# Optimization experiments

Measured on AMD Instinct MI355X. Metric: run time of the kernel, lower is better.

The kernel has to match this reference:

```python
import jax, jax.numpy as jnp
import numpy as np

NUM_HEADS = 16


def setup_inputs() -> dict:
    key = jax.random.key(0)
    k1, k2, k3 = jax.random.split(key, 3)
    B, S, D = 4, 2048, 1024
    x = jax.random.normal(k1, (B, S, D), dtype=jnp.float32)
    w_qkv = jax.random.normal(k2, (D, 3 * D), dtype=jnp.float32) * 0.02
    b_qkv = jnp.zeros((3 * D,), dtype=jnp.float32)
    w_proj = jax.random.normal(k3, (D, D), dtype=jnp.float32) * 0.02
    b_proj = jnp.zeros((D,), dtype=jnp.float32)
    return {"x": x, "w_qkv": w_qkv, "b_qkv": b_qkv, "w_proj": w_proj, "b_proj": b_proj}


def reference(x, w_qkv, b_qkv, w_proj, b_proj):
    B, S, D = x.shape
    H = NUM_HEADS
    hd = D // H
    # fused qkv projection: [B,S,3D] -> [B,S,3H,hd]
    qkv = (x @ w_qkv + b_qkv).reshape(B, S, 3 * H, hd)
    q, k, v = jnp.split(qkv, 3, axis=2)  # each [B,S,H,hd]
    scale = (1.0 / jnp.sqrt(hd)).astype(x.dtype)
    scores = jnp.einsum("bqhd,bkhd->bhqk", q, k) * scale  # [B,H,S,S]
    causal = jnp.tril(jnp.ones((S, S), dtype=bool))  # [S,S]
    masked = jnp.where(causal, scores, jnp.finfo(scores.dtype).min)
    # softmax in fp32 reduce dtype, cast back (dropout_rate=0 -> identity)
    attn = jax.nn.softmax(masked.astype(jnp.float32)).astype(masked.dtype)
    out = jnp.einsum("bhqk,bkhd->bqhd", attn, v).reshape(B, S, D)
    return out @ w_proj + b_proj
```

## Files before the change

kernel.cpp:

```cpp
#include <hip/hip_runtime.h>
#include <hip/hip_bf16.h>

typedef __attribute__((ext_vector_type(8))) short short8;
typedef __attribute__((ext_vector_type(4))) float f32x4;
typedef __attribute__((ext_vector_type(16))) float f32x16;

#define B_   4
#define S_   2048
#define D_   1024
#define H_   16
#define HD_  64
#define M_   (B_ * S_)
#define N3_  (3 * D_)

#define GLDS16(g, l)                                                        \
  __builtin_amdgcn_global_load_lds(                                         \
      (const __attribute__((address_space(1))) void*)(g),                   \
      (__attribute__((address_space(3))) void*)(l), 16, 0, 0)

__device__ __forceinline__ unsigned pack_bf2(float a, float b) {
  union { __hip_bfloat16 h; unsigned short s; } ua, ub;
  ua.h = __float2bfloat16(a);
  ub.h = __float2bfloat16(b);
  return (unsigned)ua.s | ((unsigned)ub.s << 16);
}

__global__ __launch_bounds__(256) void cast_f32_bf16(
    const float* __restrict__ in, __hip_bfloat16* __restrict__ out, int n) {
  int i = (blockIdx.x * 256 + threadIdx.x) * 4;
  if (i + 3 < n) {
    float4 v = *(const float4*)(in + i);
    union { ushort4 u4; __hip_bfloat16 h[4]; } p;
    p.h[0] = __float2bfloat16(v.x);
    p.h[1] = __float2bfloat16(v.y);
    p.h[2] = __float2bfloat16(v.z);
    p.h[3] = __float2bfloat16(v.w);
    *(ushort4*)(out + i) = p.u4;
  }
}

__global__ __launch_bounds__(256) void transpose_cast(
    const float* __restrict__ in, __hip_bfloat16* __restrict__ out,
    int rows, int cols) {
  __shared__ float tile[32][33];
  int bx = blockIdx.x * 32;
  int by = blockIdx.y * 32;
  int tx = threadIdx.x, ty = threadIdx.y;
#pragma unroll
  for (int i = 0; i < 4; ++i)
    tile[ty + i * 8][tx] = in[(size_t)(by + ty + i * 8) * cols + bx + tx];
  __syncthreads();
#pragma unroll
  for (int i = 0; i < 4; ++i)
    out[(size_t)(bx + ty + i * 8) * rows + by + tx] =
        __float2bfloat16(tile[tx][ty + i * 8]);
}

__device__ inline void store_out(float* p, float v) { *p = v; }
__device__ inline void store_out(__hip_bfloat16* p, float v) {
  *p = __float2bfloat16(v);
}

template <typename OUT_T, bool WVT>
__global__ __launch_bounds__(256) void gemm_bt_bias(
    const __hip_bfloat16* __restrict__ A, const __hip_bfloat16* __restrict__ Bt,
    const float* __restrict__ bias, OUT_T* __restrict__ C,
    __hip_bfloat16* __restrict__ vt, int M, int N, int K) {
  __shared__ __align__(16) __hip_bfloat16 Alds[128 * 64];
  __shared__ __align__(16) __hip_bfloat16 Blds[128 * 64];
  const int t = threadIdx.x;
  const int wave = t >> 6, lane = t & 63;
  const int quad = lane >> 4, l15 = lane & 15;
  const int wm = (wave >> 1) * 64, wn = (wave & 1) * 64;
  const int m0 = blockIdx.y * 128, n0 = blockIdx.x * 128;

  const int rsub = lane >> 3;
  const int gc16 = (lane & 7) ^ (rsub & 7);
  const __hip_bfloat16* gA[4];
  const __hip_bfloat16* gB[4];
  __hip_bfloat16* lA[4];
  __hip_bfloat16* lB[4];
#pragma unroll
  for (int i = 0; i < 4; ++i) {
    int c = wave * 4 + i;
    int row = c * 8 + rsub;
    gA[i] = A + (size_t)(m0 + row) * K + gc16 * 8;
    gB[i] = Bt + (size_t)(n0 + row) * K + gc16 * 8;
    lA[i] = Alds + c * 512;
    lB[i] = Blds + c * 512;
  }

  f32x4 acc[4][4] = {};

  for (int k0 = 0; k0 < K; k0 += 64) {
#pragma unroll
    for (int i = 0; i < 4; ++i) {
      GLDS16(gA[i] + k0, lA[i]);
      GLDS16(gB[i] + k0, lB[i]);
    }
    __syncthreads();
#pragma unroll
    for (int kk = 0; kk < 2; ++kk) {
      const int fo = ((kk * 4 + quad) ^ (l15 & 7)) * 8;
      short8 a[4], bfr[4];
#pragma unroll
      for (int mt = 0; mt < 4; ++mt)
        a[mt] = *(const short8*)(Alds + (wm + mt * 16 + l15) * 64 + fo);
#pragma unroll
      for (int nt = 0; nt < 4; ++nt)
        bfr[nt] = *(const short8*)(Blds + (wn + nt * 16 + l15) * 64 + fo);
#pragma unroll
      for (int mt = 0; mt < 4; ++mt)
#pragma unroll
        for (int nt = 0; nt < 4; ++nt)
          acc[mt][nt] = __builtin_amdgcn_mfma_f32_16x16x32_bf16(
              a[mt], bfr[nt], acc[mt][nt], 0, 0, 0);
    }
    __syncthreads();
  }

  if (WVT && n0 >= 2048) {
#pragma unroll
    for (int mt = 0; mt < 4; ++mt)
#pragma unroll
      for (int nt = 0; nt < 4; ++nt) {
        int col = n0 + wn + nt * 16 + l15;
        float bv = bias[col];
        int hv = (col - 2048) >> 6, d = (col - 2048) & 63;
        int row0 = m0 + wm + mt * 16 + quad * 4;
        int bidx = row0 >> 11, s = row0 & 2047;
        uint2 w;
        w.x = pack_bf2(acc[mt][nt][0] + bv, acc[mt][nt][1] + bv);
        w.y = pack_bf2(acc[mt][nt][2] + bv, acc[mt][nt][3] + bv);
        *(uint2*)(vt + ((size_t)(bidx * 16 + hv) * 64 + d) * 2048 + s) = w;
      }
  } else {
#pragma unroll
    for (int mt = 0; mt < 4; ++mt)
#pragma unroll
      for (int nt = 0; nt < 4; ++nt) {
        int col = n0 + wn + nt * 16 + l15;
        float bv = bias[col];
#pragma unroll
        for (int r = 0; r < 4; ++r) {
          int row = m0 + wm + mt * 16 + quad * 4 + r;
          store_out(C + (size_t)row * N + col, acc[mt][nt][r] + bv);
        }
      }
  }
}

__global__ __launch_bounds__(128, 2) void attn_causal(
    const __hip_bfloat16* __restrict__ qkv,
    const __hip_bfloat16* __restrict__ vt,
    __hip_bfloat16* __restrict__ ctx) {
  __shared__ __align__(16) __hip_bfloat16 Klds[2][64 * 64];
  __shared__ __align__(16) __hip_bfloat16 Vlds[2][64 * 64];

  const int t = threadIdx.x;
  const int wave = t >> 6, lane = t & 63;
  const int r31 = lane & 31, a5 = lane >> 5;
  const int xr = r31 & 7;

  const int wg = blockIdx.x;
  const int xcd = wg & 7, loc = wg >> 3;
  const int pair = (xcd << 3) | (loc >> 4);
  const int xb = loc & 15;
  const int b = pair >> 4, h = pair & 15;

  const size_t qbase = (size_t)b * S_ * N3_ + h * HD_;
  const size_t kbase = qbase + D_;
  const size_t vtbase = (size_t)(b * H_ + h) * HD_ * S_;
  const float C2 = 0.18033688f;

  short8 ones;
#pragma unroll
  for (int j = 0; j < 8; ++j) ones[j] = (short)0x3F80;

  const int rsub = lane >> 3;
  const int swz = ((lane & 7) ^ rsub) * 8;
  const __hip_bfloat16* gK[4];
  const __hip_bfloat16* gV[4];
  __hip_bfloat16* lK[4];
  __hip_bfloat16* lV[4];
#pragma unroll
  for (int i = 0; i < 4; ++i) {
    const int c = wave * 4 + i;
    gK[i] = qkv + kbase + (size_t)(c * 8 + rsub) * N3_ + swz;
    gV[i] = vt + vtbase + (size_t)(c * 8 + rsub) * S_ + swz;
    lK[i] = &Klds[0][c * 512];
    lV[i] = &Vlds[0][c * 512];
  }

#pragma unroll
  for (int i = 0; i < 4; ++i) {
    GLDS16(gK[i], lK[i]);
    GLDS16(gV[i], lV[i]);
  }
  __syncthreads();
  int cur = 0;

#define MKFRAG(sv, Bofs, OUT)                                          \
  {                                                                    \
    unsigned dA0 = pack_bf2(sv[Bofs + 0], sv[Bofs + 1]);               \
    unsigned dA1 = pack_bf2(sv[Bofs + 2], sv[Bofs + 3]);               \
    unsigned dB0 = pack_bf2(sv[Bofs + 4], sv[Bofs + 5]);               \
    unsigned dB1 = pack_bf2(sv[Bofs + 6], sv[Bofs + 7]);               \
    unsigned c0 = (unsigned)__shfl_xor((int)(a5 ? dA0 : dB0), 32);     \
    unsigned c1 = (unsigned)__shfl_xor((int)(a5 ? dA1 : dB1), 32);     \
    union { unsigned u[4]; short8 s8; } pu;                            \
    pu.u[0] = a5 ? c0 : dA0;                                           \
    pu.u[1] = a5 ? c1 : dA1;                                           \
    pu.u[2] = a5 ? dB0 : c0;                                           \
    pu.u[3] = a5 ? dB1 : c1;                                           \
    OUT = pu.s8;                                                       \
  }

  for (int sel = 0; sel < 2; ++sel) {
    const int qb = sel ? 31 - xb : xb;
    const int qrow = qb * 64 + wave * 32 + r31;
    const int rlq = wave * 32 + r31;

    short8 qf[4];
#pragma unroll
    for (int dc = 0; dc < 4; ++dc)
      qf[dc] = *(const short8*)(qkv + qbase + (size_t)qrow * N3_ +
                                dc * 16 + a5 * 8);

    f32x16 o0 = {}, o1 = {};
    float m_r = -1e30f, l_r = 0.f;

    for (int kb = 0; kb <= qb; ++kb) {
      if (sel == 0 || kb < qb) {
        const size_t nk = (kb < qb) ? (size_t)(kb + 1) : 0;
        const size_t ko = nk * (size_t)(64 * N3_);
        const size_t vo = nk * 64;
        const int nb = (cur ^ 1) * 4096;
#pragma unroll
        for (int i = 0; i < 4; ++i) {
          GLDS16(gK[i] + ko, lK[i] + nb);
          GLDS16(gV[i] + vo, lV[i] + nb);
        }
      }

      const __hip_bfloat16* Kb = &Klds[cur][0];
      const __hip_bfloat16* Vb = &Vlds[cur][0];

      short8 kf0[4], kf1[4];
#pragma unroll
      for (int dc = 0; dc < 4; ++dc) {
        const int u = ((dc * 2 + a5) ^ xr) * 8;
        kf0[dc] = *(const short8*)(Kb + r31 * 64 + u);
        kf1[dc] = *(const short8*)(Kb + (32 + r31) * 64 + u);
      }

      f32x16 s0 = {}, s1 = {};
#pragma unroll
      for (int dc = 0; dc < 4; ++dc) {
        s0 = __builtin_amdgcn_mfma_f32_32x32x16_bf16(kf0[dc], qf[dc], s0,
                                                     0, 0, 0);
        s1 = __builtin_amdgcn_mfma_f32_32x32x16_bf16(kf1[dc], qf[dc], s1,
                                                     0, 0, 0);
      }

      if (kb == qb) {
#pragma unroll
        for (int reg = 0; reg < 16; ++reg) {
          const int kl = (reg & 3) + 8 * (reg >> 2) + 4 * a5;
          if (kl > rlq) s0[reg] = -1e30f;
          if (kl + 32 > rlq) s1[reg] = -1e30f;
        }
      }

      float tm = s0[0];
#pragma unroll
      for (int reg = 1; reg < 16; ++reg) tm = fmaxf(tm, s0[reg]);
#pragma unroll
      for (int reg = 0; reg < 16; ++reg) tm = fmaxf(tm, s1[reg]);
      tm = fmaxf(tm, __shfl_xor(tm, 32));
      const float pm = tm * C2;

      if (!__all(pm - m_r <= 8.0f)) {
        const float mn = fmaxf(m_r, pm);
        const float al = __builtin_amdgcn_exp2f(m_r - mn);
        m_r = mn;
        l_r *= al;
        o0 *= al;
        o1 *= al;
      }
      const float mneg = -m_r;

#pragma unroll
      for (int reg = 0; reg < 16; ++reg) {
        s0[reg] = __builtin_amdgcn_exp2f(__builtin_fmaf(s0[reg], C2, mneg));
        s1[reg] = __builtin_amdgcn_exp2f(__builtin_fmaf(s1[reg], C2, mneg));
      }

      short8 pf[4];
      MKFRAG(s0, 0, pf[0]);
      MKFRAG(s0, 8, pf[1]);
      MKFRAG(s1, 0, pf[2]);
      MKFRAG(s1, 8, pf[3]);

      f32x16 ps = {};
#pragma unroll
      for (int kc = 0; kc < 4; ++kc)
        ps = __builtin_amdgcn_mfma_f32_32x32x16_bf16(ones, pf[kc], ps,
                                                     0, 0, 0);
      l_r += ps[0];

#pragma unroll
      for (int kc = 0; kc < 4; ++kc) {
        const int u = ((kc * 2 + a5) ^ xr) * 8;
        short8 v0 = *(const short8*)(Vb + r31 * 64 + u);
        short8 v1 = *(const short8*)(Vb + (32 + r31) * 64 + u);
        o0 = __builtin_amdgcn_mfma_f32_32x32x16_bf16(v0, pf[kc], o0, 0, 0, 0);
        o1 = __builtin_amdgcn_mfma_f32_32x32x16_bf16(v1, pf[kc], o1, 0, 0, 0);
      }

      __syncthreads();
      cur ^= 1;
    }

    const float rl = __builtin_amdgcn_rcpf(l_r);
    __hip_bfloat16* crow = ctx + ((size_t)b * S_ + qrow) * D_ + h * HD_;
#pragma unroll
    for (int q2 = 0; q2 < 4; ++q2) {
      uint2 w;
      w.x = pack_bf2(o0[q2 * 4 + 0] * rl, o0[q2 * 4 + 1] * rl);
      w.y = pack_bf2(o0[q2 * 4 + 2] * rl, o0[q2 * 4 + 3] * rl);
      *(uint2*)(crow + 8 * q2 + 4 * a5) = w;
      w.x = pack_bf2(o1[q2 * 4 + 0] * rl, o1[q2 * 4 + 1] * rl);
      w.y = pack_bf2(o1[q2 * 4 + 2] * rl, o1[q2 * 4 + 3] * rl);
      *(uint2*)(crow + 32 + 8 * q2 + 4 * a5) = w;
    }
  }
#undef MKFRAG
}

extern "C" void kernel_launch(void* const* d_in, const int* in_sizes, int n_in,
                              void* d_out, int out_size, void* d_ws,
                              size_t ws_size, hipStream_t stream) {
  const float* x      = (const float*)d_in[0];
  const float* w_qkv  = (const float*)d_in[1];
  const float* b_qkv  = (const float*)d_in[2];
  const float* w_proj = (const float*)d_in[3];
  const float* b_proj = (const float*)d_in[4];
  float* out = (float*)d_out;

  char* ws = (char*)d_ws;
  __hip_bfloat16* xb     = (__hip_bfloat16*)(ws + 0);
  __hip_bfloat16* wqkvT  = (__hip_bfloat16*)(ws + 16777216);
  __hip_bfloat16* wprojT = (__hip_bfloat16*)(ws + 23068672);
  __hip_bfloat16* qkvb   = (__hip_bfloat16*)(ws + 25165824);
  __hip_bfloat16* ctx    = (__hip_bfloat16*)(ws + 75497472);
  __hip_bfloat16* vt2    = (__hip_bfloat16*)(ws + 91750400);

  cast_f32_bf16<<<8192, 256, 0, stream>>>(x, xb, M_ * D_);
  transpose_cast<<<dim3(N3_ / 32, D_ / 32), dim3(32, 8), 0, stream>>>(
      w_qkv, wqkvT, D_, N3_);
  transpose_cast<<<dim3(D_ / 32, D_ / 32), dim3(32, 8), 0, stream>>>(
      w_proj, wprojT, D_, D_);

  gemm_bt_bias<__hip_bfloat16, true>
      <<<dim3(N3_ / 128, M_ / 128), 256, 0, stream>>>(
          xb, wqkvT, b_qkv, qkvb, vt2, M_, N3_, D_);

  attn_causal<<<1024, 128, 0, stream>>>(qkvb, vt2, ctx);

  gemm_bt_bias<float, false><<<dim3(D_ / 128, M_ / 128), 256, 0, stream>>>(
      ctx, wprojT, b_proj, out, (__hip_bfloat16*)nullptr, M_, D_, D_);
}
```

Before: 274.2 us.

## Split attention key blocks across wave pairs with LDS merge of partial softmax

Doubles the attention workgroup to four waves. Each key block's 64 keys are split into two halves handled by separate wave pairs, each keeping its own online-softmax state, and the partial outputs are merged through LDS at the end. The row sum now uses shuffles and adds instead of an MFMA against a ones vector, and the wave that covers only masked keys on the diagonal block is skipped. The aim is more waves in flight to hide latency and fewer per-wave MFMA and exp ops, at the cost of an extra reduction and syncs per query block.

```diff
diff --git a/kernel.cpp b/kernel.cpp
--- a/kernel.cpp
+++ b/kernel.cpp
@@ -150,15 +150,17 @@
   }
 }
 
-__global__ __launch_bounds__(128, 2) void attn_causal(
+__global__ __launch_bounds__(256, 4) void attn_causal(
     const __hip_bfloat16* __restrict__ qkv,
     const __hip_bfloat16* __restrict__ vt,
     __hip_bfloat16* __restrict__ ctx) {
   __shared__ __align__(16) __hip_bfloat16 Klds[2][64 * 64];
   __shared__ __align__(16) __hip_bfloat16 Vlds[2][64 * 64];
+  __shared__ float mlbuf[64][2];
 
   const int t = threadIdx.x;
   const int wave = t >> 6, lane = t & 63;
+  const int kh = wave >> 1, rh = wave & 1;
   const int r31 = lane & 31, a5 = lane >> 5;
   const int xr = r31 & 7;
 
@@ -173,19 +175,15 @@
   const size_t vtbase = (size_t)(b * H_ + h) * HD_ * S_;
   const float C2 = 0.18033688f;
 
-  short8 ones;
-#pragma unroll
-  for (int j = 0; j < 8; ++j) ones[j] = (short)0x3F80;
-
   const int rsub = lane >> 3;
   const int swz = ((lane & 7) ^ rsub) * 8;
-  const __hip_bfloat16* gK[4];
-  const __hip_bfloat16* gV[4];
-  __hip_bfloat16* lK[4];
-  __hip_bfloat16* lV[4];
-#pragma unroll
-  for (int i = 0; i < 4; ++i) {
-    const int c = wave * 4 + i;
+  const __hip_bfloat16* gK[2];
+  const __hip_bfloat16* gV[2];
+  __hip_bfloat16* lK[2];
+  __hip_bfloat16* lV[2];
+#pragma unroll
+  for (int i = 0; i < 2; ++i) {
+    const int c = wave * 2 + i;
     gK[i] = qkv + kbase + (size_t)(c * 8 + rsub) * N3_ + swz;
     gV[i] = vt + vtbase + (size_t)(c * 8 + rsub) * S_ + swz;
     lK[i] = &Klds[0][c * 512];
@@ -193,7 +191,7 @@
   }
 
 #pragma unroll
-  for (int i = 0; i < 4; ++i) {
+  for (int i = 0; i < 2; ++i) {
     GLDS16(gK[i], lK[i]);
     GLDS16(gV[i], lV[i]);
   }
@@ -218,8 +216,7 @@
 
   for (int sel = 0; sel < 2; ++sel) {
     const int qb = sel ? 31 - xb : xb;
-    const int qrow = qb * 64 + wave * 32 + r31;
-    const int rlq = wave * 32 + r31;
+    const int qrow = qb * 64 + rh * 32 + r31;
 
     short8 qf[4];
 #pragma unroll
@@ -237,103 +234,142 @@
         const size_t vo = nk * 64;
         const int nb = (cur ^ 1) * 4096;
 #pragma unroll
-        for (int i = 0; i < 4; ++i) {
+        for (int i = 0; i < 2; ++i) {
           GLDS16(gK[i] + ko, lK[i] + nb);
           GLDS16(gV[i] + vo, lV[i] + nb);
         }
       }
 
-      const __hip_bfloat16* Kb = &Klds[cur][0];
-      const __hip_bfloat16* Vb = &Vlds[cur][0];
-
-      short8 kf0[4], kf1[4];
-#pragma unroll
-      for (int dc = 0; dc < 4; ++dc) {
-        const int u = ((dc * 2 + a5) ^ xr) * 8;
-        kf0[dc] = *(const short8*)(Kb + r31 * 64 + u);
-        kf1[dc] = *(const short8*)(Kb + (32 + r31) * 64 + u);
-      }
-
-      f32x16 s0 = {}, s1 = {};
-#pragma unroll
-      for (int dc = 0; dc < 4; ++dc) {
-        s0 = __builtin_amdgcn_mfma_f32_32x32x16_bf16(kf0[dc], qf[dc], s0,
-                                                     0, 0, 0);
-        s1 = __builtin_amdgcn_mfma_f32_32x32x16_bf16(kf1[dc], qf[dc], s1,
-                                                     0, 0, 0);
-      }
-
-      if (kb == qb) {
-#pragma unroll
-        for (int reg = 0; reg < 16; ++reg) {
-          const int kl = (reg & 3) + 8 * (reg >> 2) + 4 * a5;
-          if (kl > rlq) s0[reg] = -1e30f;
-          if (kl + 32 > rlq) s1[reg] = -1e30f;
+      const bool diag = (kb == qb);
+      if (!(diag && kh == 1 && rh == 0)) {
+        const __hip_bfloat16* Kb = &Klds[cur][0];
+        const __hip_bfloat16* Vb = &Vlds[cur][0];
+
+        short8 kf[4];
+#pragma unroll
+        for (int dc = 0; dc < 4; ++dc)
+          kf[dc] = *(const short8*)(Kb + (kh * 32 + r31) * 64 +
+                                    (((dc * 2 + a5) ^ xr) * 8));
+
+        f32x16 s = {};
+#pragma unroll
+        for (int dc = 0; dc < 4; ++dc)
+          s = __builtin_amdgcn_mfma_f32_32x32x16_bf16(kf[dc], qf[dc], s,
+                                                      0, 0, 0);
+
+        if (diag && kh == rh) {
+#pragma unroll
+          for (int reg = 0; reg < 16; ++reg) {
+            const int kin = (reg & 3) + 8 * (reg >> 2) + 4 * a5;
+            if (kin > r31) s[reg] = -1e30f;
+          }
         }
-      }
-
-      float tm = s0[0];
-#pragma unroll
-      for (int reg = 1; reg < 16; ++reg) tm = fmaxf(tm, s0[reg]);
-#pragma unroll
-      for (int reg = 0; reg < 16; ++reg) tm = fmaxf(tm, s1[reg]);
-      tm = fmaxf(tm, __shfl_xor(tm, 32));
-      const float pm = tm * C2;
-
-      if (!__all(pm - m_r <= 8.0f)) {
-        const float mn = fmaxf(m_r, pm);
-        const float al = __builtin_amdgcn_exp2f(m_r - mn);
-        m_r = mn;
-        l_r *= al;
-        o0 *= al;
-        o1 *= al;
-      }
-      const float mneg = -m_r;
-
-#pragma unroll
-      for (int reg = 0; reg < 16; ++reg) {
-        s0[reg] = __builtin_amdgcn_exp2f(__builtin_fmaf(s0[reg], C2, mneg));
-        s1[reg] = __builtin_amdgcn_exp2f(__builtin_fmaf(s1[reg], C2, mneg));
-      }
-
-      short8 pf[4];
-      MKFRAG(s0, 0, pf[0]);
-      MKFRAG(s0, 8, pf[1]);
-      MKFRAG(s1, 0, pf[2]);
-      MKFRAG(s1, 8, pf[3]);
-
-      f32x16 ps = {};
-#pragma unroll
-      for (int kc = 0; kc < 4; ++kc)
-        ps = __builtin_amdgcn_mfma_f32_32x32x16_bf16(ones, pf[kc], ps,
-                                                     0, 0, 0);
-      l_r += ps[0];
-
-#pragma unroll
-      for (int kc = 0; kc < 4; ++kc) {
-        const int u = ((kc * 2 + a5) ^ xr) * 8;
-        short8 v0 = *(const short8*)(Vb + r31 * 64 + u);
-        short8 v1 = *(const short8*)(Vb + (32 + r31) * 64 + u);
-        o0 = __builtin_amdgcn_mfma_f32_32x32x16_bf16(v0, pf[kc], o0, 0, 0, 0);
-        o1 = __builtin_amdgcn_mfma_f32_32x32x16_bf16(v1, pf[kc], o1, 0, 0, 0);
+
+        float t8[8];
+#pragma unroll
+        for (int i = 0; i < 8; ++i) t8[i] = fmaxf(s[i], s[i + 8]);
+#pragma unroll
+        for (int st = 4; st >= 1; st >>= 1)
+#pragma unroll
+          for (int i = 0; i < 4; ++i)
+            if (i < st) t8[i] = fmaxf(t8[i], t8[i + st]);
+        float tm = fmaxf(t8[0], __shfl_xor(t8[0], 32));
+        const float pm = tm * C2;
+
+        if (!__all(pm - m_r <= 8.0f)) {
+          const float mn = fmaxf(m_r, pm);
+          const float al = __builtin_amdgcn_exp2f(m_r - mn);
+          m_r = mn;
+          l_r *= al;
+          o0 *= al;
+          o1 *= al;
+        }
+        const float mneg = -m_r;
+
+#pragma unroll
+        for (int reg = 0; reg < 16; ++reg)
+          s[reg] = __builtin_amdgcn_exp2f(__builtin_fmaf(s[reg], C2, mneg));
+
+        float u8[8];
+#pragma unroll
+        for (int i = 0; i < 8; ++i) u8[i] = s[i] + s[i + 8];
+#pragma unroll
+        for (int st = 4; st >= 1; st >>= 1)
+#pragma unroll
+          for (int i = 0; i < 4; ++i)
+            if (i < st) u8[i] = u8[i] + u8[i + st];
+        l_r += u8[0] + __shfl_xor(u8[0], 32);
+
+        short8 pf[2];
+        MKFRAG(s, 0, pf[0]);
+        MKFRAG(s, 8, pf[1]);
+
+#pragma unroll
+        for (int kc = 0; kc < 2; ++kc) {
+          const int u = (((kh * 2 + kc) * 2 + a5) ^ xr) * 8;
+          short8 v0 = *(const short8*)(Vb + r31 * 64 + u);
+          short8 v1 = *(const short8*)(Vb + (32 + r31) * 64 + u);
+          o0 = __builtin_amdgcn_mfma_f32_32x32x16_bf16(v0, pf[kc], o0,
+                                                       0, 0, 0);
+          o1 = __builtin_amdgcn_mfma_f32_32x32x16_bf16(v1, pf[kc], o1,
+                                                       0, 0, 0);
+        }
       }
 
       __syncthreads();
       cur ^= 1;
     }
 
-    const float rl = __builtin_amdgcn_rcpf(l_r);
-    __hip_bfloat16* crow = ctx + ((size_t)b * S_ + qrow) * D_ + h * HD_;
-#pragma unroll
-    for (int q2 = 0; q2 < 4; ++q2) {
-      uint2 w;
-      w.x = pack_bf2(o0[q2 * 4 + 0] * rl, o0[q2 * 4 + 1] * rl);
-      w.y = pack_bf2(o0[q2 * 4 + 2] * rl, o0[q2 * 4 + 3] * rl);
-      *(uint2*)(crow + 8 * q2 + 4 * a5) = w;
-      w.x = pack_bf2(o1[q2 * 4 + 0] * rl, o1[q2 * 4 + 1] * rl);
-      w.y = pack_bf2(o1[q2 * 4 + 2] * rl, o1[q2 * 4 + 3] * rl);
-      *(uint2*)(crow + 32 + 8 * q2 + 4 * a5) = w;
+    if (kh == 1) {
+      if (a5 == 0) {
+        mlbuf[rh * 32 + r31][0] = m_r;
+        mlbuf[rh * 32 + r31][1] = l_r;
+      }
+      float* obase =
+          (rh ? (float*)&Vlds[cur ^ 1][0] : (float*)&Klds[cur ^ 1][0]) +
+          r31 * 64;
+#pragma unroll
+      for (int q2 = 0; q2 < 4; ++q2) {
+        float4 w0 = {o0[q2 * 4 + 0], o0[q2 * 4 + 1],
+                     o0[q2 * 4 + 2], o0[q2 * 4 + 3]};
+        *(float4*)(obase + 8 * q2 + 4 * a5) = w0;
+        float4 w1 = {o1[q2 * 4 + 0], o1[q2 * 4 + 1],
+                     o1[q2 * 4 + 2], o1[q2 * 4 + 3]};
+        *(float4*)(obase + 32 + 8 * q2 + 4 * a5) = w1;
+      }
     }
+    __syncthreads();
+    if (kh == 0) {
+      const float m_b = mlbuf[rh * 32 + r31][0];
+      const float l_b = mlbuf[rh * 32 + r31][1];
+      const float mn = fmaxf(m_r, m_b);
+      const float aa = __builtin_amdgcn_exp2f(m_r - mn);
+      const float ab = __builtin_amdgcn_exp2f(m_b - mn);
+      const float lt = l_r * aa + l_b * ab;
+      const float rl = __builtin_amdgcn_rcpf(lt);
+      const float fa = aa * rl, fb = ab * rl;
+      const float* obase =
+          (rh ? (const float*)&Vlds[cur ^ 1][0]
+              : (const float*)&Klds[cur ^ 1][0]) + r31 * 64;
+      __hip_bfloat16* crow = ctx + ((size_t)b * S_ + qrow) * D_ + h * HD_;
+#pragma unroll
+      for (int q2 = 0; q2 < 4; ++q2) {
+        float4 vb0 = *(const float4*)(obase + 8 * q2 + 4 * a5);
+        float4 vb1 = *(const float4*)(obase + 32 + 8 * q2 + 4 * a5);
+        uint2 w;
+        w.x = pack_bf2(o0[q2 * 4 + 0] * fa + vb0.x * fb,
+                       o0[q2 * 4 + 1] * fa + vb0.y * fb);
+        w.y = pack_bf2(o0[q2 * 4 + 2] * fa + vb0.z * fb,
+                       o0[q2 * 4 + 3] * fa + vb0.w * fb);
+        *(uint2*)(crow + 8 * q2 + 4 * a5) = w;
+        w.x = pack_bf2(o1[q2 * 4 + 0] * fa + vb1.x * fb,
+                       o1[q2 * 4 + 1] * fa + vb1.y * fb);
+        w.y = pack_bf2(o1[q2 * 4 + 2] * fa + vb1.z * fb,
+                       o1[q2 * 4 + 3] * fa + vb1.w * fb);
+        *(uint2*)(crow + 32 + 8 * q2 + 4 * a5) = w;
+      }
+    }
+    __syncthreads();
   }
 #undef MKFRAG
 }
@@ -366,7 +402,7 @@
       <<<dim3(N3_ / 128, M_ / 128), 256, 0, stream>>>(
           xb, wqkvT, b_qkv, qkvb, vt2, M_, N3_, D_);
 
-  attn_causal<<<1024, 128, 0, stream>>>(qkvb, vt2, ctx);
+  attn_causal<<<1024, 256, 0, stream>>>(qkvb, vt2, ctx);
 
   gemm_bt_bias<float, false><<<dim3(D_ / 128, M_ / 128), 256, 0, stream>>>(
       ctx, wprojT, b_proj, out, (__hip_bfloat16*)nullptr, M_, D_, D_);
```

Measured after the change: 266.8 us. 1.03x faster.
